# Kernel optimization log

Measured on AMD Instinct MI355X. Metric: run time of the kernel, lower is better.

Reference implementation:

```python
import jax, jax.numpy as jnp
import numpy as np

N_NODES = 1_000_000
N_GRAPHS = 1024
DIM = 128


def setup_inputs() -> dict:
    key = jax.random.key(0)
    k1, k2, k3, k4 = jax.random.split(key, 4)
    h = jax.random.normal(k1, (N_NODES, DIM), dtype=jnp.float32)
    vn_h = jax.random.normal(k2, (N_GRAPHS, DIM), dtype=jnp.float32)
    segment_ids = jnp.sort(jax.random.randint(k3, (N_NODES,), 0, N_GRAPHS, dtype=jnp.int32))
    W = jax.random.normal(k4, (DIM, DIM), dtype=jnp.float32) * (1.0 / np.sqrt(DIM))
    b = jnp.zeros((DIM,), dtype=jnp.float32)
    return {"h": h, "vn_h": vn_h, "segment_ids": segment_ids, "W": W, "b": b}


def reference(h, vn_h, segment_ids, W, b):
    # per-graph mean pool (mean_nodes): segment sum / segment count
    sums = jax.ops.segment_sum(h, segment_ids, num_segments=N_GRAPHS)          # [G, dim]
    counts = jax.ops.segment_sum(jnp.ones((h.shape[0],), h.dtype), segment_ids,
                                 num_segments=N_GRAPHS)                        # [G]
    pool = sums / jnp.maximum(counts, 1.0)[:, None]                            # [G, dim]
    # FCLayer: Linear + ReLU (dropout=0, batch_norm=False -> identity)
    vn_h_temp = jax.nn.relu((vn_h + pool) @ W + b)                             # [G, dim]
    # residual update of virtual node state
    vn_h_new = vn_h + vn_h_temp                                                # [G, dim]
    # broadcast virtual node back to its graph's nodes (ragged repeat == gather)
    h_new = h + vn_h_new[segment_ids]                                          # [N, dim]
    return (vn_h_new, h_new)
```

## Files before the change

### kernel.cpp

```cpp
#include <hip/hip_runtime.h>

#define DIM 128
#define CAP 512
#define MAXT 12
#define NTHREADS 1024

typedef float fx4 __attribute__((ext_vector_type(4)));

#define STAGE_BYTES (CAP * 32 * 8)
#define RED_BYTES   (16 * 32 * 16)
#define SMEM_BYTES  (STAGE_BYTES + RED_BYTES + 2 * DIM * 4 + 16)

__device__ __forceinline__ unsigned bfr(float f) {
    unsigned u = __float_as_uint(f);
    return (u + 0x7fffu + ((u >> 16) & 1u)) >> 16;
}
__device__ __forceinline__ uint2 pack4(fx4 v) {
    return make_uint2(bfr(v.x) | (bfr(v.y) << 16), bfr(v.z) | (bfr(v.w) << 16));
}
__device__ __forceinline__ fx4 unpack4(uint2 u) {
    fx4 r;
    r.x = __uint_as_float(u.x << 16);
    r.y = __uint_as_float(u.x & 0xffff0000u);
    r.z = __uint_as_float(u.y << 16);
    r.w = __uint_as_float(u.y & 0xffff0000u);
    return r;
}

__device__ __forceinline__ int lb_search(const int* __restrict__ seg, int n, int val) {
    int lo = 0, hi = n;
    while (lo < hi) {
        int mid = (lo + hi) >> 1;
        if (seg[mid] < val) lo = mid + 1; else hi = mid;
    }
    return lo;
}

__global__ void k_offsets(const int* __restrict__ seg, int* __restrict__ offs,
                          int n, int ngraphs) {
    const int i = blockIdx.x * blockDim.x + threadIdx.x;
    if (i >= n) return;
    const int a = seg[i];
    if (i == 0) {
        for (int g = 0; g <= a; ++g) offs[g] = 0;
    } else {
        const int p = seg[i - 1];
        for (int g = p + 1; g <= a; ++g) offs[g] = i;
    }
    if (i == n - 1) {
        for (int g = a + 1; g <= ngraphs; ++g) offs[g] = n;
    }
}

__global__ __launch_bounds__(NTHREADS, 4) void k_fused(
        const float* __restrict__ h, const float* __restrict__ vn_h,
        const int* __restrict__ seg, const float* __restrict__ W,
        const float* __restrict__ bias, const int* __restrict__ offs,
        float* __restrict__ vn_out, float* __restrict__ h_out,
        int N, int G) {
    extern __shared__ char smem[];
    uint2* stage = (uint2*)smem;
    fx4*   red   = (fx4*)(smem + STAGE_BYTES);
    float* wred  = (float*)(smem + STAGE_BYTES);
    float* xs    = (float*)(smem + STAGE_BYTES + RED_BYTES);
    float* vns   = xs + DIM;
    int*   bnd   = (int*)(vns + DIM);

    const int g   = blockIdx.x;
    const int tid = threadIdx.x;
    const int tx  = tid & 31;
    const int ty  = tid >> 5;

    if (offs) {
        if (tid < 2) bnd[tid] = offs[g + tid];
    } else {
        if (tid < 2) bnd[tid] = lb_search(seg, N, g + tid);
    }
    __syncthreads();
    const int rs = bnd[0];
    const int re = bnd[1];
    const int n  = re - rs;

    fx4 a0 = {0.f,0.f,0.f,0.f}, a1 = {0.f,0.f,0.f,0.f};
    const int lim1 = min(rs + CAP, re);
    {
        int r = rs + ty;
        for (; r + 32 < lim1; r += 64) {
            const fx4 v0 = *(const fx4*)(h + (size_t)r        * DIM + tx * 4);
            const fx4 v1 = *(const fx4*)(h + (size_t)(r + 32) * DIM + tx * 4);
            a0 += v0; a1 += v1;
            stage[(r - rs)      * 32 + tx] = pack4(v0);
            stage[(r - rs + 32) * 32 + tx] = pack4(v1);
        }
        if (r < lim1) {
            const fx4 v = *(const fx4*)(h + (size_t)r * DIM + tx * 4);
            a0 += v;
            stage[(r - rs) * 32 + tx] = pack4(v);
        }
    }

    fx4 tl[MAXT];
    const int tb = rs + CAP;
    #pragma unroll
    for (int j = 0; j < MAXT; ++j) {
        const int rr = tb + j * 32 + ty;
        fx4 v = {0.f, 0.f, 0.f, 0.f};
        if (rr < re) v = *(const fx4*)(h + (size_t)rr * DIM + tx * 4);
        tl[j] = v;
        a1 += v;
    }

    for (int r = tb + MAXT * 32 + ty; r < re; r += 32)
        a0 += *(const fx4*)(h + (size_t)r * DIM + tx * 4);

    a0 += a1;
    fx4 t = a0;
    t.x += __shfl_xor(a0.x, 32);
    t.y += __shfl_xor(a0.y, 32);
    t.z += __shfl_xor(a0.z, 32);
    t.w += __shfl_xor(a0.w, 32);
    if ((tid & 32) == 0) red[(ty >> 1) * 32 + tx] = t;
    __syncthreads();

    if (tid < 32) {
        fx4 p2 = red[tx];
        #pragma unroll
        for (int w = 1; w < 16; ++w) p2 += red[w * 32 + tx];
        const float inv = 1.0f / (float)max(n, 1);
        const fx4 vnh = *(const fx4*)(vn_h + (size_t)g * DIM + tx * 4);
        *(fx4*)(xs + tx * 4) = vnh + p2 * inv;
    }
    __syncthreads();

    {
        const int d    = tid & (DIM - 1);
        const int part = tid >> 7;
        const int k0   = part * (DIM / 8);
        float dp = 0.f;
        #pragma unroll
        for (int k = 0; k < DIM / 8; ++k)
            dp = fmaf(xs[k0 + k], W[(size_t)(k0 + k) * DIM + d], dp);
        wred[d * 9 + part] = dp;
    }
    __syncthreads();
    if (tid < DIM) {
        float dot = bias[tid];
        #pragma unroll
        for (int p = 0; p < 8; ++p) dot += wred[tid * 9 + p];
        const float vn = vn_h[(size_t)g * DIM + tid] + fmaxf(dot, 0.0f);
        vns[tid] = vn;
        vn_out[(size_t)g * DIM + tid] = vn;
    }
    __syncthreads();

    {
        const fx4 vnv = *(const fx4*)(vns + tx * 4);
        int r = rs + ty;
        for (; r + 32 < lim1; r += 64) {
            const int l0 = r - rs;
            __builtin_nontemporal_store(
                unpack4(stage[l0 * 32 + tx]) + vnv,
                (fx4*)(h_out + (size_t)r * DIM + tx * 4));
            __builtin_nontemporal_store(
                unpack4(stage[(l0 + 32) * 32 + tx]) + vnv,
                (fx4*)(h_out + (size_t)(r + 32) * DIM + tx * 4));
        }
        if (r < lim1) {
            __builtin_nontemporal_store(
                unpack4(stage[(r - rs) * 32 + tx]) + vnv,
                (fx4*)(h_out + (size_t)r * DIM + tx * 4));
        }
        #pragma unroll
        for (int j = 0; j < MAXT; ++j) {
            const int rr = tb + j * 32 + ty;
            if (rr < re)
                __builtin_nontemporal_store(
                    tl[j] + vnv, (fx4*)(h_out + (size_t)rr * DIM + tx * 4));
        }
        for (int r2 = tb + MAXT * 32 + ty; r2 < re; r2 += 32) {
            const fx4 hv = *(const fx4*)(h + (size_t)r2 * DIM + tx * 4);
            __builtin_nontemporal_store(
                hv + vnv, (fx4*)(h_out + (size_t)r2 * DIM + tx * 4));
        }
    }
}

extern "C" void kernel_launch(void* const* d_in, const int* in_sizes, int n_in,
                              void* d_out, int out_size, void* d_ws, size_t ws_size,
                              hipStream_t stream) {
    const float* h    = (const float*)d_in[0];
    const float* vn_h = (const float*)d_in[1];
    const int*   seg  = (const int*)d_in[2];
    const float* W    = (const float*)d_in[3];
    const float* bias = (const float*)d_in[4];

    int N = in_sizes[0] / DIM;
    int G = in_sizes[1] / DIM;

    float* vn_out = (float*)d_out;
    float* h_out  = vn_out + (size_t)G * DIM;

    int* offs = nullptr;
    if (ws_size >= (size_t)(G + 1) * sizeof(int)) {
        offs = (int*)d_ws;
        hipLaunchKernelGGL(k_offsets, dim3((N + 255) / 256), dim3(256), 0,
                           stream, seg, offs, N, G);
    }

    hipFuncSetAttribute((const void*)k_fused,
                        hipFuncAttributeMaxDynamicSharedMemorySize, SMEM_BYTES);

    hipLaunchKernelGGL(k_fused, dim3(G), dim3(NTHREADS), SMEM_BYTES, stream,
                       h, vn_h, seg, W, bias, offs, vn_out, h_out, N, G);
}
```

Baseline: 202.3 us.

## Make fused kernel persistent and overlap next graph's loads with previous graph's stores

Launches a fixed grid of 256 blocks that each loop over graphs, software-pipelining so that the loads and reduction for graph k run interleaved with writing h_out for graph k-1 from the bf16 LDS stage and register tail. This targets the serialized read-then-write phases within each block and the cost of per-graph block launch. In exchange, only 256 blocks of 1024 threads run, which may leave CUs underoccupied on a 256-CU device. The staging buffer is reused in place, so a slot is read for the previous graph before it is overwritten by the current one.

```diff
diff --git a/kernel.cpp b/kernel.cpp
--- a/kernel.cpp
+++ b/kernel.cpp
@@ -4,6 +4,7 @@
 #define CAP 512
 #define MAXT 12
 #define NTHREADS 1024
+#define NB 256
 
 typedef float fx4 __attribute__((ext_vector_type(4)));
 
@@ -66,98 +67,151 @@
     float* vns   = xs + DIM;
     int*   bnd   = (int*)(vns + DIM);
 
-    const int g   = blockIdx.x;
+    const int b   = blockIdx.x;
     const int tid = threadIdx.x;
     const int tx  = tid & 31;
     const int ty  = tid >> 5;
 
-    if (offs) {
-        if (tid < 2) bnd[tid] = offs[g + tid];
-    } else {
-        if (tid < 2) bnd[tid] = lb_search(seg, N, g + tid);
-    }
-    __syncthreads();
-    const int rs = bnd[0];
-    const int re = bnd[1];
-    const int n  = re - rs;
-
-    fx4 a0 = {0.f,0.f,0.f,0.f}, a1 = {0.f,0.f,0.f,0.f};
-    const int lim1 = min(rs + CAP, re);
+    fx4 tl[MAXT];
+    fx4 vnv_p = {0.f, 0.f, 0.f, 0.f};
+    int rs_p = 0, re_p = 0, tb_p = 0;
+
+    const int rounds = (G + NB - 1) / NB;
+    for (int k = 0; k < rounds; ++k) {
+        const int g = k * NB + b;
+        int rs = 0, re = 0;
+        if (g < G) {
+            if (offs) {
+                rs = offs[g];
+                re = offs[g + 1];
+            } else {
+                if (tid < 2) bnd[tid] = lb_search(seg, N, g + tid);
+                __syncthreads();
+                rs = bnd[0];
+                re = bnd[1];
+            }
+        }
+        const int n    = re - rs;
+        const int lim1 = min(rs + CAP, re);
+        const int tb   = rs + CAP;
+
+        fx4 a0 = {0.f,0.f,0.f,0.f}, a1 = {0.f,0.f,0.f,0.f};
+
+        if (k == 0) {
+            int r = rs + ty;
+            for (; r + 32 < lim1; r += 64) {
+                const fx4 v0 = *(const fx4*)(h + (size_t)r        * DIM + tx * 4);
+                const fx4 v1 = *(const fx4*)(h + (size_t)(r + 32) * DIM + tx * 4);
+                a0 += v0; a1 += v1;
+                stage[(r - rs)      * 32 + tx] = pack4(v0);
+                stage[(r - rs + 32) * 32 + tx] = pack4(v1);
+            }
+            if (r < lim1) {
+                const fx4 v = *(const fx4*)(h + (size_t)r * DIM + tx * 4);
+                a0 += v;
+                stage[(r - rs) * 32 + tx] = pack4(v);
+            }
+            #pragma unroll
+            for (int j = 0; j < MAXT; ++j) {
+                const int rr = tb + j * 32 + ty;
+                fx4 v = {0.f, 0.f, 0.f, 0.f};
+                if (rr < re) v = *(const fx4*)(h + (size_t)rr * DIM + tx * 4);
+                tl[j] = v;
+                a1 += v;
+            }
+            for (int r2 = tb + MAXT * 32 + ty; r2 < re; r2 += 32)
+                a0 += *(const fx4*)(h + (size_t)r2 * DIM + tx * 4);
+        } else {
+            const int np = re_p - rs_p;
+            #pragma unroll 2
+            for (int c = 0; c < CAP / 32; ++c) {
+                const int l  = c * 32 + ty;
+                const int rc = rs + l;
+                const int rp = rs_p + l;
+                const bool ldc = (rc < lim1);
+                fx4 v = {0.f, 0.f, 0.f, 0.f};
+                if (ldc) v = *(const fx4*)(h + (size_t)rc * DIM + tx * 4);
+                if (l < np) {
+                    const fx4 o = unpack4(stage[l * 32 + tx]) + vnv_p;
+                    __builtin_nontemporal_store(
+                        o, (fx4*)(h_out + (size_t)rp * DIM + tx * 4));
+                }
+                if (ldc) { stage[l * 32 + tx] = pack4(v); a0 += v; }
+            }
+            #pragma unroll
+            for (int j = 0; j < MAXT; ++j) {
+                const int rp = tb_p + j * 32 + ty;
+                const int rc = tb   + j * 32 + ty;
+                if (rp < re_p)
+                    __builtin_nontemporal_store(
+                        tl[j] + vnv_p, (fx4*)(h_out + (size_t)rp * DIM + tx * 4));
+                fx4 v = {0.f, 0.f, 0.f, 0.f};
+                if (rc < re) {
+                    v = *(const fx4*)(h + (size_t)rc * DIM + tx * 4);
+                    a1 += v;
+                }
+                tl[j] = v;
+            }
+            for (int rp = tb_p + MAXT * 32 + ty; rp < re_p; rp += 32) {
+                const fx4 hv = *(const fx4*)(h + (size_t)rp * DIM + tx * 4);
+                __builtin_nontemporal_store(
+                    hv + vnv_p, (fx4*)(h_out + (size_t)rp * DIM + tx * 4));
+            }
+            for (int rc = tb + MAXT * 32 + ty; rc < re; rc += 32)
+                a0 += *(const fx4*)(h + (size_t)rc * DIM + tx * 4);
+        }
+
+        a0 += a1;
+        fx4 t = a0;
+        t.x += __shfl_xor(a0.x, 32);
+        t.y += __shfl_xor(a0.y, 32);
+        t.z += __shfl_xor(a0.z, 32);
+        t.w += __shfl_xor(a0.w, 32);
+        if ((tid & 32) == 0) red[(ty >> 1) * 32 + tx] = t;
+        __syncthreads();
+        if (tid < 32) {
+            fx4 p2 = red[tx];
+            #pragma unroll
+            for (int w = 1; w < 16; ++w) p2 += red[w * 32 + tx];
+            const float inv = 1.0f / (float)max(n, 1);
+            fx4 vnh = {0.f, 0.f, 0.f, 0.f};
+            if (g < G) vnh = *(const fx4*)(vn_h + (size_t)g * DIM + tx * 4);
+            *(fx4*)(xs + tx * 4) = vnh + p2 * inv;
+        }
+        __syncthreads();
+
+        {
+            const int d    = tid & (DIM - 1);
+            const int part = tid >> 7;
+            const int k0   = part * (DIM / 8);
+            float dp = 0.f;
+            #pragma unroll
+            for (int kk = 0; kk < DIM / 8; ++kk)
+                dp = fmaf(xs[k0 + kk], W[(size_t)(k0 + kk) * DIM + d], dp);
+            wred[d * 9 + part] = dp;
+        }
+        __syncthreads();
+        if (tid < DIM) {
+            float dot = bias[tid];
+            #pragma unroll
+            for (int p = 0; p < 8; ++p) dot += wred[tid * 9 + p];
+            float vh = 0.f;
+            if (g < G) vh = vn_h[(size_t)g * DIM + tid];
+            const float vn = vh + fmaxf(dot, 0.0f);
+            vns[tid] = vn;
+            if (g < G) vn_out[(size_t)g * DIM + tid] = vn;
+        }
+        __syncthreads();
+        vnv_p = *(const fx4*)(vns + tx * 4);
+        rs_p = rs; re_p = re; tb_p = tb;
+    }
+
     {
-        int r = rs + ty;
-        for (; r + 32 < lim1; r += 64) {
-            const fx4 v0 = *(const fx4*)(h + (size_t)r        * DIM + tx * 4);
-            const fx4 v1 = *(const fx4*)(h + (size_t)(r + 32) * DIM + tx * 4);
-            a0 += v0; a1 += v1;
-            stage[(r - rs)      * 32 + tx] = pack4(v0);
-            stage[(r - rs + 32) * 32 + tx] = pack4(v1);
-        }
-        if (r < lim1) {
-            const fx4 v = *(const fx4*)(h + (size_t)r * DIM + tx * 4);
-            a0 += v;
-            stage[(r - rs) * 32 + tx] = pack4(v);
-        }
-    }
-
-    fx4 tl[MAXT];
-    const int tb = rs + CAP;
-    #pragma unroll
-    for (int j = 0; j < MAXT; ++j) {
-        const int rr = tb + j * 32 + ty;
-        fx4 v = {0.f, 0.f, 0.f, 0.f};
-        if (rr < re) v = *(const fx4*)(h + (size_t)rr * DIM + tx * 4);
-        tl[j] = v;
-        a1 += v;
-    }
-
-    for (int r = tb + MAXT * 32 + ty; r < re; r += 32)
-        a0 += *(const fx4*)(h + (size_t)r * DIM + tx * 4);
-
-    a0 += a1;
-    fx4 t = a0;
-    t.x += __shfl_xor(a0.x, 32);
-    t.y += __shfl_xor(a0.y, 32);
-    t.z += __shfl_xor(a0.z, 32);
-    t.w += __shfl_xor(a0.w, 32);
-    if ((tid & 32) == 0) red[(ty >> 1) * 32 + tx] = t;
-    __syncthreads();
-
-    if (tid < 32) {
-        fx4 p2 = red[tx];
-        #pragma unroll
-        for (int w = 1; w < 16; ++w) p2 += red[w * 32 + tx];
-        const float inv = 1.0f / (float)max(n, 1);
-        const fx4 vnh = *(const fx4*)(vn_h + (size_t)g * DIM + tx * 4);
-        *(fx4*)(xs + tx * 4) = vnh + p2 * inv;
-    }
-    __syncthreads();
-
-    {
-        const int d    = tid & (DIM - 1);
-        const int part = tid >> 7;
-        const int k0   = part * (DIM / 8);
-        float dp = 0.f;
-        #pragma unroll
-        for (int k = 0; k < DIM / 8; ++k)
-            dp = fmaf(xs[k0 + k], W[(size_t)(k0 + k) * DIM + d], dp);
-        wred[d * 9 + part] = dp;
-    }
-    __syncthreads();
-    if (tid < DIM) {
-        float dot = bias[tid];
-        #pragma unroll
-        for (int p = 0; p < 8; ++p) dot += wred[tid * 9 + p];
-        const float vn = vn_h[(size_t)g * DIM + tid] + fmaxf(dot, 0.0f);
-        vns[tid] = vn;
-        vn_out[(size_t)g * DIM + tid] = vn;
-    }
-    __syncthreads();
-
-    {
-        const fx4 vnv = *(const fx4*)(vns + tx * 4);
-        int r = rs + ty;
-        for (; r + 32 < lim1; r += 64) {
-            const int l0 = r - rs;
+        const int lim1p = min(rs_p + CAP, re_p);
+        const fx4 vnv = vnv_p;
+        int r = rs_p + ty;
+        for (; r + 32 < lim1p; r += 64) {
+            const int l0 = r - rs_p;
             __builtin_nontemporal_store(
                 unpack4(stage[l0 * 32 + tx]) + vnv,
                 (fx4*)(h_out + (size_t)r * DIM + tx * 4));
@@ -165,22 +219,21 @@
                 unpack4(stage[(l0 + 32) * 32 + tx]) + vnv,
                 (fx4*)(h_out + (size_t)(r + 32) * DIM + tx * 4));
         }
-        if (r < lim1) {
-            __builtin_nontemporal_store(
-                unpack4(stage[(r - rs) * 32 + tx]) + vnv,
+        if (r < lim1p)
+            __builtin_nontemporal_store(
+                unpack4(stage[(r - rs_p) * 32 + tx]) + vnv,
                 (fx4*)(h_out + (size_t)r * DIM + tx * 4));
-        }
         #pragma unroll
         for (int j = 0; j < MAXT; ++j) {
-            const int rr = tb + j * 32 + ty;
-            if (rr < re)
+            const int rp = tb_p + j * 32 + ty;
+            if (rp < re_p)
                 __builtin_nontemporal_store(
-                    tl[j] + vnv, (fx4*)(h_out + (size_t)rr * DIM + tx * 4));
-        }
-        for (int r2 = tb + MAXT * 32 + ty; r2 < re; r2 += 32) {
-            const fx4 hv = *(const fx4*)(h + (size_t)r2 * DIM + tx * 4);
-            __builtin_nontemporal_store(
-                hv + vnv, (fx4*)(h_out + (size_t)r2 * DIM + tx * 4));
+                    tl[j] + vnv, (fx4*)(h_out + (size_t)rp * DIM + tx * 4));
+        }
+        for (int rp = tb_p + MAXT * 32 + ty; rp < re_p; rp += 32) {
+            const fx4 hv = *(const fx4*)(h + (size_t)rp * DIM + tx * 4);
+            __builtin_nontemporal_store(
+                hv + vnv, (fx4*)(h_out + (size_t)rp * DIM + tx * 4));
         }
     }
 }
@@ -210,6 +263,6 @@
     hipFuncSetAttribute((const void*)k_fused,
                         hipFuncAttributeMaxDynamicSharedMemorySize, SMEM_BYTES);
 
-    hipLaunchKernelGGL(k_fused, dim3(G), dim3(NTHREADS), SMEM_BYTES, stream,
+    hipLaunchKernelGGL(k_fused, dim3(NB), dim3(NTHREADS), SMEM_BYTES, stream,
                        h, vn_h, seg, W, bias, offs, vn_out, h_out, N, G);
 }
```

Result: slower. 233.8 us (+15.6%).
